# Kernel optimization log

Measured on AMD Instinct MI355X. Metric: run time of the kernel, lower is better.

## Reference

```python
import jax, jax.numpy as jnp
import numpy as np

B, N, K = 4, 40960, 16
D_OUT = 16
BN_EPS = 1e-5


def setup_inputs() -> dict:
    key = jax.random.key(0)
    k1, k2, k3, k4 = jax.random.split(key, 4)
    xyz = jax.random.normal(k1, (B, N, 3), dtype=jnp.float32)
    feature = jax.random.normal(k2, (B, N, 8), dtype=jnp.float32)
    neigh_idx = jax.random.randint(k3, (B, N, K), 0, N, dtype=jnp.int64)
    # Conv2d(10, d_out, (1,1), bn=True): conv weight [d_out, 10], no bias, BN params
    W = jax.random.normal(k4, (D_OUT, 10), dtype=jnp.float32) * 0.1
    gamma = jnp.ones((D_OUT,), dtype=jnp.float32)
    beta = jnp.zeros((D_OUT,), dtype=jnp.float32)
    running_mean = jnp.zeros((D_OUT,), dtype=jnp.float32)
    running_var = jnp.ones((D_OUT,), dtype=jnp.float32)
    return {"xyz": xyz, "feature": feature, "neigh_idx": neigh_idx,
            "W": W, "gamma": gamma, "beta": beta,
            "running_mean": running_mean, "running_var": running_var}


def reference(xyz, feature, neigh_idx, W, gamma, beta, running_mean, running_var):
    # gather_neighbour: [B, N, K, 3]
    neighbor_xyz = jnp.take_along_axis(xyz[:, :, None, :],
                                       neigh_idx[:, :, :, None], axis=1)
    xyz_tile = jnp.broadcast_to(xyz[:, :, None, :], neighbor_xyz.shape)
    relative_xyz = xyz_tile - neighbor_xyz
    relative_dis = jnp.sqrt(jnp.sum(relative_xyz * relative_xyz, axis=-1, keepdims=True))
    # [B, N, K, 10]
    f_xyz = jnp.concatenate([relative_dis, relative_xyz, xyz_tile, neighbor_xyz], axis=-1)
    # 1x1 conv over channel dim (10 -> d_out), then eval-mode BN + ReLU
    y = jnp.einsum('bnkc,oc->bonk', f_xyz, W)  # [B, d_out, N, K]
    inv_std = jax.lax.rsqrt(running_var + BN_EPS)
    scale = (gamma * inv_std)[None, :, None, None]
    shift = (beta - gamma * running_mean * inv_std)[None, :, None, None]
    return jax.nn.relu(y * scale + shift)
```

## Files before the change

### kernel.cpp

```cpp
#include <hip/hip_runtime.h>

#define BB 4
#define NN 40960
#define KK 16
#define DOUT 16
#define BN_EPS 1e-5f

typedef float f32x4 __attribute__((ext_vector_type(4)));

__global__ __launch_bounds__(256) void Block_72464688218281_kernel(
    const float* __restrict__ xyz,
    const int*   __restrict__ nidx,
    const float* __restrict__ W,
    const float* __restrict__ gamma,
    const float* __restrict__ beta,
    const float* __restrict__ rmean,
    const float* __restrict__ rvar,
    float* __restrict__ out)
{
    __shared__ f32x4 Pc[DOUT];
    __shared__ f32x4 Pn[DOUT];
    if (threadIdx.x < DOUT) {
        const int o = threadIdx.x;
        const float istd = rsqrtf(rvar[o] + BN_EPS);
        const float sc   = gamma[o] * istd;
        const float sh   = beta[o] - gamma[o] * rmean[o] * istd;
        const float w0 = W[o * 10 + 0], w1 = W[o * 10 + 1], w2 = W[o * 10 + 2];
        const float w3 = W[o * 10 + 3], w4 = W[o * 10 + 4], w5 = W[o * 10 + 5];
        const float w6 = W[o * 10 + 6], w7 = W[o * 10 + 7], w8 = W[o * 10 + 8];
        const float w9 = W[o * 10 + 9];
        f32x4 pc; pc.x = w0 * sc;        pc.y = (w1 + w4) * sc;
                  pc.z = (w2 + w5) * sc; pc.w = (w3 + w6) * sc;
        f32x4 pn; pn.x = (w7 - w1) * sc; pn.y = (w8 - w2) * sc;
                  pn.z = (w9 - w3) * sc; pn.w = sh;
        Pc[o] = pc;
        Pn[o] = pn;
    }
    __syncthreads();

    const int t = blockIdx.x * blockDim.x + threadIdx.x;
    if (t >= BB * NN * (KK / 4)) return;

    const int kq = t & 3;
    const int bn = t >> 2;
    const int b  = bn / NN;
    const int n  = bn - b * NN;

    const int4 i4 = *(const int4*)(nidx + (size_t)bn * KK + kq * 4);

    const float* cp = xyz + (size_t)bn * 3;
    const float cx = cp[0], cy = cp[1], cz = cp[2];

    const float* xb = xyz + (size_t)b * NN * 3;
    int ids[4] = { i4.x, i4.y, i4.z, i4.w };

    float ax[4], ay[4], az[4], dd[4];
#pragma unroll
    for (int j = 0; j < 4; ++j) {
        const float* p = xb + (size_t)ids[j] * 3;
        const float nx = p[0], ny = p[1], nz = p[2];
        ax[j] = nx; ay[j] = ny; az[j] = nz;
        const float dx = cx - nx, dy = cy - ny, dz = cz - nz;
        dd[j] = sqrtf(dx * dx + dy * dy + dz * dz);
    }

    float* ob = out + (size_t)b * DOUT * NN * KK + (size_t)n * KK + kq * 4;

#pragma unroll 4
    for (int o = 0; o < DOUT; ++o) {
        const f32x4 pc = Pc[o];
        const f32x4 pn = Pn[o];
        const float base = pn.w + pc.y * cx + pc.z * cy + pc.w * cz;

        f32x4 r;
        r.x = fmaxf(base + pc.x * dd[0] + pn.x * ax[0] + pn.y * ay[0] + pn.z * az[0], 0.0f);
        r.y = fmaxf(base + pc.x * dd[1] + pn.x * ax[1] + pn.y * ay[1] + pn.z * az[1], 0.0f);
        r.z = fmaxf(base + pc.x * dd[2] + pn.x * ax[2] + pn.y * ay[2] + pn.z * az[2], 0.0f);
        r.w = fmaxf(base + pc.x * dd[3] + pn.x * ax[3] + pn.y * ay[3] + pn.z * az[3], 0.0f);

        __builtin_nontemporal_store(r, (f32x4*)(ob + (size_t)o * NN * KK));
    }
}

extern "C" void kernel_launch(void* const* d_in, const int* in_sizes, int n_in,
                              void* d_out, int out_size, void* d_ws, size_t ws_size,
                              hipStream_t stream) {
    const float* xyz   = (const float*)d_in[0];
    const int*   nidx  = (const int*)d_in[2];
    const float* W     = (const float*)d_in[3];
    const float* gamma = (const float*)d_in[4];
    const float* beta  = (const float*)d_in[5];
    const float* rmean = (const float*)d_in[6];
    const float* rvar  = (const float*)d_in[7];
    float* out = (float*)d_out;

    const int total  = BB * NN * (KK / 4);
    const int block  = 256;
    const int grid   = (total + block - 1) / block;
    Block_72464688218281_kernel<<<grid, block, 0, stream>>>(
        xyz, nidx, W, gamma, beta, rmean, rvar, out);
}
```

Measured before the change: 200.4 us.

## Stage output tiles in LDS and compute folded weights per thread

Each block now writes its results for 8 output channels into a shared-memory staging buffer. After a barrier, each wave writes two channels' contiguous 4 KB rows of output, repeated for two channel halves. The shared-memory parameter setup and its barrier are replaced by per-thread recomputation of the folded BN/conv coefficients from uniform loads. The stores also drop the nontemporal hint, and the bounds check is removed on the assumption that the grid divides exactly. The aim is more contiguous write streams per wave, at the cost of extra LDS traffic and two barriers per half.

Result: no change. 197.3 us (-1.5%).

```diff
diff --git a/kernel.cpp b/kernel.cpp
--- a/kernel.cpp
+++ b/kernel.cpp
@@ -18,33 +18,15 @@
     const float* __restrict__ rvar,
     float* __restrict__ out)
 {
-    __shared__ f32x4 Pc[DOUT];
-    __shared__ f32x4 Pn[DOUT];
-    if (threadIdx.x < DOUT) {
-        const int o = threadIdx.x;
-        const float istd = rsqrtf(rvar[o] + BN_EPS);
-        const float sc   = gamma[o] * istd;
-        const float sh   = beta[o] - gamma[o] * rmean[o] * istd;
-        const float w0 = W[o * 10 + 0], w1 = W[o * 10 + 1], w2 = W[o * 10 + 2];
-        const float w3 = W[o * 10 + 3], w4 = W[o * 10 + 4], w5 = W[o * 10 + 5];
-        const float w6 = W[o * 10 + 6], w7 = W[o * 10 + 7], w8 = W[o * 10 + 8];
-        const float w9 = W[o * 10 + 9];
-        f32x4 pc; pc.x = w0 * sc;        pc.y = (w1 + w4) * sc;
-                  pc.z = (w2 + w5) * sc; pc.w = (w3 + w6) * sc;
-        f32x4 pn; pn.x = (w7 - w1) * sc; pn.y = (w8 - w2) * sc;
-                  pn.z = (w9 - w3) * sc; pn.w = sh;
-        Pc[o] = pc;
-        Pn[o] = pn;
-    }
-    __syncthreads();
+    __shared__ f32x4 stage[8][256];
 
-    const int t = blockIdx.x * blockDim.x + threadIdx.x;
-    if (t >= BB * NN * (KK / 4)) return;
+    const int tid = threadIdx.x;
+    const int t   = blockIdx.x * 256 + tid;
 
     const int kq = t & 3;
     const int bn = t >> 2;
     const int b  = bn / NN;
-    const int n  = bn - b * NN;
+    const int n0 = (blockIdx.x * 64) % NN;
 
     const int4 i4 = *(const int4*)(nidx + (size_t)bn * KK + kq * 4);
 
@@ -52,7 +34,7 @@
     const float cx = cp[0], cy = cp[1], cz = cp[2];
 
     const float* xb = xyz + (size_t)b * NN * 3;
-    int ids[4] = { i4.x, i4.y, i4.z, i4.w };
+    const int ids[4] = { i4.x, i4.y, i4.z, i4.w };
 
     float ax[4], ay[4], az[4], dd[4];
 #pragma unroll
@@ -64,21 +46,47 @@
         dd[j] = sqrtf(dx * dx + dy * dy + dz * dz);
     }
 
-    float* ob = out + (size_t)b * DOUT * NN * KK + (size_t)n * KK + kq * 4;
+    const int wid  = tid >> 6;
+    const int lane = tid & 63;
 
-#pragma unroll 4
-    for (int o = 0; o < DOUT; ++o) {
-        const f32x4 pc = Pc[o];
-        const f32x4 pn = Pn[o];
-        const float base = pn.w + pc.y * cx + pc.z * cy + pc.w * cz;
+#pragma unroll
+    for (int h = 0; h < 2; ++h) {
+#pragma unroll
+        for (int oo = 0; oo < 8; ++oo) {
+            const int o = h * 8 + oo;
+            const float istd = rsqrtf(rvar[o] + BN_EPS);
+            const float sc   = gamma[o] * istd;
+            const float sh   = beta[o] - gamma[o] * rmean[o] * istd;
+            const float pcx = W[o*10+0] * sc;
+            const float ux  = (W[o*10+1] + W[o*10+4]) * sc;
+            const float uy  = (W[o*10+2] + W[o*10+5]) * sc;
+            const float uz  = (W[o*10+3] + W[o*10+6]) * sc;
+            const float vx  = (W[o*10+7] - W[o*10+1]) * sc;
+            const float vy  = (W[o*10+8] - W[o*10+2]) * sc;
+            const float vz  = (W[o*10+9] - W[o*10+3]) * sc;
+            const float base = sh + ux * cx + uy * cy + uz * cz;
 
-        f32x4 r;
-        r.x = fmaxf(base + pc.x * dd[0] + pn.x * ax[0] + pn.y * ay[0] + pn.z * az[0], 0.0f);
-        r.y = fmaxf(base + pc.x * dd[1] + pn.x * ax[1] + pn.y * ay[1] + pn.z * az[1], 0.0f);
-        r.z = fmaxf(base + pc.x * dd[2] + pn.x * ax[2] + pn.y * ay[2] + pn.z * az[2], 0.0f);
-        r.w = fmaxf(base + pc.x * dd[3] + pn.x * ax[3] + pn.y * ay[3] + pn.z * az[3], 0.0f);
+            f32x4 r;
+            r.x = fmaxf(base + pcx * dd[0] + vx * ax[0] + vy * ay[0] + vz * az[0], 0.0f);
+            r.y = fmaxf(base + pcx * dd[1] + vx * ax[1] + vy * ay[1] + vz * az[1], 0.0f);
+            r.z = fmaxf(base + pcx * dd[2] + vx * ax[2] + vy * ay[2] + vz * az[2], 0.0f);
+            r.w = fmaxf(base + pcx * dd[3] + vx * ax[3] + vy * ay[3] + vz * az[3], 0.0f);
+            stage[oo][tid] = r;
+        }
+        __syncthreads();
 
-        __builtin_nontemporal_store(r, (f32x4*)(ob + (size_t)o * NN * KK));
+#pragma unroll
+        for (int q = 0; q < 2; ++q) {
+            const int oo = wid * 2 + q;
+            const int o  = h * 8 + oo;
+            float* pb = out + ((size_t)(b * DOUT + o) * NN + n0) * KK;
+#pragma unroll
+            for (int c = 0; c < 4; ++c) {
+                const f32x4 v = stage[oo][c * 64 + lane];
+                *(f32x4*)(pb + (size_t)(c * 64 + lane) * 4) = v;
+            }
+        }
+        __syncthreads();
     }
 }
 
@@ -94,9 +102,9 @@
     const float* rvar  = (const float*)d_in[7];
     float* out = (float*)d_out;
 
-    const int total  = BB * NN * (KK / 4);
-    const int block  = 256;
-    const int grid   = (total + block - 1) / block;
+    const int total = BB * NN * (KK / 4);
+    const int block = 256;
+    const int grid  = total / block;
     Block_72464688218281_kernel<<<grid, block, 0, stream>>>(
         xyz, nidx, W, gamma, beta, rmean, rvar, out);
 }
```
